# Optimization experiments

Measured on AMD Instinct MI355X. Metric: run time of the kernel, lower is better.

## Reference

```python
import jax, jax.numpy as jnp
import numpy as np

N_EMBED = 1024
HEAD_SIZE = 64


def setup_inputs() -> dict:
    key = jax.random.key(0)
    kx, kk, kq, kv = jax.random.split(key, 4)
    B, T = 8, 2048
    x = jax.random.normal(kx, (B, T, N_EMBED), dtype=jnp.float32)
    # nn.Linear weights, stored as (in, out) so projection is x @ W
    s = 1.0 / np.sqrt(N_EMBED)
    Wk = jax.random.uniform(kk, (N_EMBED, HEAD_SIZE), jnp.float32, -s, s)
    Wq = jax.random.uniform(kq, (N_EMBED, HEAD_SIZE), jnp.float32, -s, s)
    Wv = jax.random.uniform(kv, (N_EMBED, HEAD_SIZE), jnp.float32, -s, s)
    return {"x": x, "Wk": Wk, "Wq": Wq, "Wv": Wv}


def reference(x, Wk, Wq, Wv):
    # x: [B, T, C] with C = n_embed
    C = x.shape[-1]
    k = x @ Wk  # [B, T, H]
    q = x @ Wq  # [B, T, H]
    v = x @ Wv  # [B, T, H]
    # NOTE: original scales by n_embed**-0.5, not head_size**-0.5
    wei = jnp.einsum("bth,bsh->bts", q, k) * (C ** -0.5)  # [B, T, T]
    wei = jax.nn.softmax(wei, axis=-1)
    # dropout = 0.0 (eval mode) -> identity
    out = jnp.einsum("bts,bsh->bth", wei, v)  # [B, T, H]
    return out
```

## Files before the change

kernel.cpp:

```cpp
#include <hip/hip_runtime.h>
#include <stdint.h>


#define B_ 8
#define T_ 2048
#define C_ 1024
#define H_ 64

typedef float f32x4 __attribute__((ext_vector_type(4)));
typedef short s16x8 __attribute__((ext_vector_type(8)));

__device__ __forceinline__ unsigned int rhu16(float f) {
    return (__float_as_uint(f) + 0x8000u) >> 16;
}
__device__ __forceinline__ unsigned int pkbf(float lo, float hi) {
    unsigned int a = __float_as_uint(lo) + 0x8000u;
    unsigned int b = __float_as_uint(hi) + 0x8000u;
    return __builtin_amdgcn_perm(b, a, 0x07060302u);
}
__device__ __forceinline__ void ld_lds16(const void* g, void* l) {
    __builtin_amdgcn_global_load_lds(
        (const __attribute__((address_space(1))) unsigned int*)g,
        (__attribute__((address_space(3))) unsigned int*)l, 16, 0, 0);
}

__global__ __launch_bounds__(256) void wconv(const float* __restrict__ Wk,
        const float* __restrict__ Wq, const float* __restrict__ Wv,
        unsigned short* __restrict__ Wt) {
    __shared__ float ls[64 * 65];
    const int bx = blockIdx.x, t = threadIdx.x;
    const int mat = bx >> 4, c0 = (bx & 15) << 6;
    const float* W = (mat == 0) ? Wk : ((mat == 1) ? Wq : Wv);
    const float sc = (mat == 1) ? 0.03125f : 1.0f;
    #pragma unroll
    for (int k = 0; k < 4; k++) {
        int i = t + (k << 8);
        int cr = i >> 4, hq = (i & 15) << 2;
        float4 v = *reinterpret_cast<const float4*>(&W[(size_t)(c0 + cr) * H_ + hq]);
        ls[cr * 65 + hq + 0] = v.x; ls[cr * 65 + hq + 1] = v.y;
        ls[cr * 65 + hq + 2] = v.z; ls[cr * 65 + hq + 3] = v.w;
    }
    __syncthreads();
    #pragma unroll
    for (int k = 0; k < 4; k++) {
        int i = t + (k << 8);
        int h = i >> 4, cq = (i & 15) << 2;
        float a = ls[(cq + 0) * 65 + h] * sc, b = ls[(cq + 1) * 65 + h] * sc;
        float c = ls[(cq + 2) * 65 + h] * sc, d = ls[(cq + 3) * 65 + h] * sc;
        uint2 o; o.x = pkbf(a, b); o.y = pkbf(c, d);
        *reinterpret_cast<uint2*>(&Wt[(size_t)(mat * 64 + h) * C_ + c0 + cq]) = o;
    }
}

__global__ __launch_bounds__(256, 2) void qkv(const float* __restrict__ x,
        const unsigned short* __restrict__ Wt,
        unsigned short* __restrict__ kb, unsigned short* __restrict__ qb,
        unsigned short* __restrict__ vtb) {
    __shared__ __align__(16) char smem[65536];
    char* xb = smem;
    char* wb = smem + 16384;

    const int t = threadIdx.x, lane = t & 63, w = t >> 6;
    const int l15 = lane & 15, quad = lane >> 4;
    const int bx = blockIdx.x;
    const int bb = bx >> 6;
    const int mt = ((bx & 7) << 3) | ((bx >> 3) & 7);
    const int m0 = bb * T_ + mt * 32;
    const int colb = w * 48;

    size_t xg[2]; int xl[2];
    #pragma unroll
    for (int n = 0; n < 2; n++) {
        int id = w * 2 + n, rg = id >> 2, j = id & 3;
        xg[n] = (size_t)(m0 + rg * 16 + l15) * C_ + j * 16 + quad * 4;
        xl[n] = id * 1024 + lane * 16;
    }
    size_t wg[6]; int wl[6];
    #pragma unroll
    for (int n = 0; n < 6; n++) {
        int g = w * 6 + n;
        wg[n] = (size_t)(g * 8 + (lane & 7)) * C_ + (lane >> 3) * 8;
        wl[n] = g * 1024 + lane * 16;
    }

    #pragma unroll
    for (int n = 0; n < 2; n++) ld_lds16(x + xg[n], xb + xl[n]);
    #pragma unroll
    for (int n = 0; n < 6; n++) ld_lds16(Wt + wg[n], wb + wl[n]);
    __syncthreads();

    f32x4 acc[2][3];
    #pragma unroll
    for (int rt = 0; rt < 2; rt++)
        #pragma unroll
        for (int ct = 0; ct < 3; ct++)
            #pragma unroll
            for (int j = 0; j < 4; j++) acc[rt][ct][j] = 0.0f;

    #pragma unroll
    for (int i = 0; i < 16; i++) {
        const int cb = i & 1;
        const float* xc = (const float*)(xb + cb * 8192);
        const unsigned short* wc = (const unsigned short*)(wb + cb * 24576);

        float4 xr[2][2][2];
        #pragma unroll
        for (int rt = 0; rt < 2; rt++)
            #pragma unroll
            for (int ks = 0; ks < 2; ks++)
                #pragma unroll
                for (int h = 0; h < 2; h++) {
                    int c = ks * 32 + quad * 8 + h * 4;
                    int j = c >> 4, u = (c & 15) >> 2;
                    xr[rt][ks][h] = *reinterpret_cast<const float4*>(
                        xc + (rt * 4 + j) * 256 + u * 64 + l15 * 4);
                }
        s16x8 wfr[3][2];
        #pragma unroll
        for (int ct = 0; ct < 3; ct++)
            #pragma unroll
            for (int ks = 0; ks < 2; ks++) {
                int col = colb + ct * 16 + l15;
                wfr[ct][ks] = *reinterpret_cast<const s16x8*>(
                    wc + (col >> 3) * 512 + ((4 * ks + quad) * 8 + (col & 7)) * 8);
            }

        if (i < 15) {
            const int c1 = (i + 1) * 64;
            char* xn = xb + (cb ^ 1) * 8192;
            char* wn = wb + (cb ^ 1) * 24576;
            #pragma unroll
            for (int n = 0; n < 2; n++) ld_lds16(x + xg[n] + c1, xn + xl[n]);
            #pragma unroll
            for (int n = 0; n < 6; n++) ld_lds16(Wt + wg[n] + c1, wn + wl[n]);
        }

        s16x8 af[2][2];
        #pragma unroll
        for (int rt = 0; rt < 2; rt++)
            #pragma unroll
            for (int ks = 0; ks < 2; ks++) {
                const float4 a = xr[rt][ks][0], b = xr[rt][ks][1];
                uint4 pk;
                pk.x = pkbf(a.x, a.y); pk.y = pkbf(a.z, a.w);
                pk.z = pkbf(b.x, b.y); pk.w = pkbf(b.z, b.w);
                af[rt][ks] = *reinterpret_cast<s16x8*>(&pk);
            }
        #pragma unroll
        for (int ks = 0; ks < 2; ks++)
            #pragma unroll
            for (int rt = 0; rt < 2; rt++)
                #pragma unroll
                for (int ct = 0; ct < 3; ct++)
                    acc[rt][ct] = __builtin_amdgcn_mfma_f32_16x16x32_bf16(
                        af[rt][ks], wfr[ct][ks], acc[rt][ct], 0, 0, 0);
        __syncthreads();
    }

    #pragma unroll
    for (int ct = 0; ct < 3; ct++) {
        int cbv = colb + ct * 16;
        int sel = cbv >> 6;
        int h = (cbv & 63) + l15;
        #pragma unroll
        for (int rt = 0; rt < 2; rt++) {
            int row0 = m0 + rt * 16 + quad * 4;
            if (sel < 2) {
                unsigned short* dst = sel ? qb : kb;
                #pragma unroll
                for (int r = 0; r < 4; r++)
                    dst[(size_t)(row0 + r) * H_ + h] = (unsigned short)rhu16(acc[rt][ct][r]);
            } else {
                int tt = row0 - bb * T_;
                uint2 pk;
                pk.x = pkbf(acc[rt][ct][0], acc[rt][ct][1]);
                pk.y = pkbf(acc[rt][ct][2], acc[rt][ct][3]);
                *reinterpret_cast<uint2*>(&vtb[((size_t)bb * H_ + h) * T_ + tt]) = pk;
            }
        }
    }
}

__global__ __launch_bounds__(256, 2) void attn(
        const unsigned short* __restrict__ qb,
        const unsigned short* __restrict__ kb,
        const unsigned short* __restrict__ vtb,
        float* __restrict__ out) {
    __shared__ __align__(16) char smem[75776];

    const int t = threadIdx.x, lane = t & 63, w = t >> 6;
    const int l15 = lane & 15, quad = lane >> 4;
    const int bb = blockIdx.x & 7;
    const int q0 = (blockIdx.x >> 3) << 5;
    const size_t kbase = (size_t)bb * T_ * H_;
    char* Kb = smem + w * 16384;
    char* Vb = Kb + 8192;
    unsigned short* Pw = (unsigned short*)(smem + 65536 + w * 2560);

    s16x8 qf[2][2];
    #pragma unroll
    for (int rt = 0; rt < 2; rt++)
        #pragma unroll
        for (int ks = 0; ks < 2; ks++)
            qf[rt][ks] = *reinterpret_cast<const s16x8*>(
                &qb[kbase + (size_t)(q0 + rt * 16 + l15) * H_ + ks * 32 + quad * 8]);

    const unsigned short* kp = kb + kbase;
    const unsigned short* vp = vtb + (size_t)bb * H_ * T_;
    size_t kg[4], vg[4]; int kl[4], vl[4];
    #pragma unroll
    for (int g = 0; g < 4; g++) {
        kg[g] = (size_t)(g * 8 + (lane & 7)) * H_ + (lane >> 3) * 8;
        kl[g] = g * 1024 + lane * 16;
        vg[g] = (size_t)(g * 16 + l15) * T_ + quad * 8;
        vl[g] = g * 1024 + lane * 16;
    }

    const int sw = w << 9;
    #pragma unroll
    for (int g = 0; g < 4; g++) ld_lds16(kp + (size_t)sw * H_ + kg[g], Kb + kl[g]);
    #pragma unroll
    for (int g = 0; g < 4; g++) ld_lds16(vp + sw + vg[g], Vb + vl[g]);

    f32x4 oacc[2][4];
    #pragma unroll
    for (int rt = 0; rt < 2; rt++)
        #pragma unroll
        for (int ht = 0; ht < 4; ht++)
            #pragma unroll
            for (int j = 0; j < 4; j++) oacc[rt][ht][j] = 0.0f;
    float l_run[2] = {0.0f, 0.0f};
    const f32x4 z4 = {0.0f, 0.0f, 0.0f, 0.0f};

    for (int it = 0; it < 16; it++) {
        const int cb = it & 1;
        __builtin_amdgcn_s_waitcnt(0x0f70);
        const unsigned short* Kc = (const unsigned short*)(Kb + cb * 4096);
        const unsigned short* Vc = (const unsigned short*)(Vb + cb * 4096);

        s16x8 kf[2][2], vf[4];
        #pragma unroll
        for (int st = 0; st < 2; st++)
            #pragma unroll
            for (int ks = 0; ks < 2; ks++) {
                int s = st * 16 + l15;
                kf[st][ks] = *reinterpret_cast<const s16x8*>(
                    Kc + (s >> 3) * 512 + ((4 * ks + quad) * 8 + (s & 7)) * 8);
            }
        #pragma unroll
        for (int ht = 0; ht < 4; ht++)
            vf[ht] = *reinterpret_cast<const s16x8*>(
                Vc + ht * 512 + (quad * 16 + l15) * 8);

        if (it < 15) {
            const int sn = sw + (it + 1) * 32;
            char* Kn = Kb + (cb ^ 1) * 4096;
            char* Vn = Vb + (cb ^ 1) * 4096;
            #pragma unroll
            for (int g = 0; g < 4; g++) ld_lds16(kp + (size_t)sn * H_ + kg[g], Kn + kl[g]);
            #pragma unroll
            for (int g = 0; g < 4; g++) ld_lds16(vp + sn + vg[g], Vn + vl[g]);
        }

        f32x4 sacc[2][2];
        #pragma unroll
        for (int rt = 0; rt < 2; rt++)
            #pragma unroll
            for (int st = 0; st < 2; st++) {
                f32x4 s0v = __builtin_amdgcn_mfma_f32_16x16x32_bf16(kf[st][0], qf[rt][0], z4, 0, 0, 0);
                sacc[rt][st] = __builtin_amdgcn_mfma_f32_16x16x32_bf16(kf[st][1], qf[rt][1], s0v, 0, 0, 0);
            }

        #pragma unroll
        for (int rt = 0; rt < 2; rt++) {
            float ls = 0.0f;
            #pragma unroll
            for (int st = 0; st < 2; st++) {
                float p0 = __expf(sacc[rt][st][0]);
                float p1 = __expf(sacc[rt][st][1]);
                float p2 = __expf(sacc[rt][st][2]);
                float p3 = __expf(sacc[rt][st][3]);
                ls += (p0 + p1) + (p2 + p3);
                uint2 pk; pk.x = pkbf(p0, p1); pk.y = pkbf(p2, p3);
                *reinterpret_cast<uint2*>(
                    &Pw[(rt * 16 + l15) * 40 + st * 16 + quad * 4]) = pk;
            }
            l_run[rt] += ls;
        }

        #pragma unroll
        for (int rt = 0; rt < 2; rt++) {
            s16x8 pf = *reinterpret_cast<const s16x8*>(&Pw[(rt * 16 + l15) * 40 + quad * 8]);
            #pragma unroll
            for (int ht = 0; ht < 4; ht++)
                oacc[rt][ht] = __builtin_amdgcn_mfma_f32_16x16x32_bf16(
                    pf, vf[ht], oacc[rt][ht], 0, 0, 0);
        }
    }

    #pragma unroll
    for (int rt = 0; rt < 2; rt++) {
        l_run[rt] += __shfl_xor(l_run[rt], 16);
        l_run[rt] += __shfl_xor(l_run[rt], 32);
    }

    __syncthreads();
    float* Osf = (float*)smem;
    float* Ls  = (float*)smem + 3 * 32 * 66;
    if (w > 0) {
        int wi = w - 1;
        #pragma unroll
        for (int rt = 0; rt < 2; rt++) {
            if (quad == 0) Ls[wi * 32 + rt * 16 + l15] = l_run[rt];
            #pragma unroll
            for (int ht = 0; ht < 4; ht++)
                #pragma unroll
                for (int r = 0; r < 4; r++)
                    Osf[wi * 2112 + (rt * 16 + quad * 4 + r) * 66 + ht * 16 + l15] = oacc[rt][ht][r];
        }
    }
    __syncthreads();
    if (w == 0) {
        #pragma unroll
        for (int rt = 0; rt < 2; rt++)
            #pragma unroll
            for (int r = 0; r < 4; r++) {
                int row = rt * 16 + quad * 4 + r;
                float lt = __shfl(l_run[rt], quad * 4 + r)
                         + Ls[0 * 32 + row] + Ls[1 * 32 + row] + Ls[2 * 32 + row];
                float inv = 1.0f / lt;
                #pragma unroll
                for (int ht = 0; ht < 4; ht++) {
                    float o = oacc[rt][ht][r]
                            + Osf[0 * 2112 + row * 66 + ht * 16 + l15]
                            + Osf[1 * 2112 + row * 66 + ht * 16 + l15]
                            + Osf[2 * 2112 + row * 66 + ht * 16 + l15];
                    out[kbase + (size_t)(q0 + row) * H_ + ht * 16 + l15] = o * inv;
                }
            }
    }
}

extern "C" void kernel_launch(void* const* d_in, const int* in_sizes, int n_in,
                              void* d_out, int out_size, void* d_ws, size_t ws_size,
                              hipStream_t stream) {
    const float* x  = (const float*)d_in[0];
    const float* Wk = (const float*)d_in[1];
    const float* Wq = (const float*)d_in[2];
    const float* Wv = (const float*)d_in[3];

    unsigned short* kb  = (unsigned short*)d_ws;
    unsigned short* qbf = kb  + (size_t)B_ * T_ * H_;
    unsigned short* vtb = qbf + (size_t)B_ * T_ * H_;
    unsigned short* Wt  = (unsigned short*)d_out;

    wconv<<<48,  256, 0, stream>>>(Wk, Wq, Wv, Wt);
    qkv  <<<512, 256, 0, stream>>>(x, Wt, kb, qbf, vtb);
    attn <<<512, 256, 0, stream>>>(qbf, kb, vtb, (float*)d_out);
}
```

Baseline: 153.3 us.

## Load QKV operands straight to registers and issue attention prefetch earlier

The QKV projection kernel drops its LDS double buffering. It now uses 128-thread blocks where each wave computes 96 output columns, loading x rows and bf16 weight fragments from global memory straight into registers. A three-slot register prefetch ring over the x chunks replaces the per-iteration `__syncthreads`. In the attention kernel, the next K/V tile's async LDS loads are issued before the wait, and the waitcnt is relaxed to let those newer loads stay in flight, so copy overlaps compute. Trade-offs: more registers and repeated weight reads from L2 in the projection, and reliance on per-wave buffer ownership to make the reordered attention prefetch safe.

```diff
diff --git a/kernel.cpp b/kernel.cpp
--- a/kernel.cpp
+++ b/kernel.cpp
@@ -52,95 +52,76 @@
     }
 }
 
-__global__ __launch_bounds__(256, 2) void qkv(const float* __restrict__ x,
+__global__ __launch_bounds__(128, 2) void qkv(const float* __restrict__ x,
         const unsigned short* __restrict__ Wt,
         unsigned short* __restrict__ kb, unsigned short* __restrict__ qb,
         unsigned short* __restrict__ vtb) {
-    __shared__ __align__(16) char smem[65536];
-    char* xb = smem;
-    char* wb = smem + 16384;
-
     const int t = threadIdx.x, lane = t & 63, w = t >> 6;
     const int l15 = lane & 15, quad = lane >> 4;
-    const int bx = blockIdx.x;
-    const int bb = bx >> 6;
-    const int mt = ((bx & 7) << 3) | ((bx >> 3) & 7);
-    const int m0 = bb * T_ + mt * 32;
-    const int colb = w * 48;
-
-    size_t xg[2]; int xl[2];
-    #pragma unroll
-    for (int n = 0; n < 2; n++) {
-        int id = w * 2 + n, rg = id >> 2, j = id & 3;
-        xg[n] = (size_t)(m0 + rg * 16 + l15) * C_ + j * 16 + quad * 4;
-        xl[n] = id * 1024 + lane * 16;
-    }
-    size_t wg[6]; int wl[6];
-    #pragma unroll
-    for (int n = 0; n < 6; n++) {
-        int g = w * 6 + n;
-        wg[n] = (size_t)(g * 8 + (lane & 7)) * C_ + (lane >> 3) * 8;
-        wl[n] = g * 1024 + lane * 16;
-    }
-
-    #pragma unroll
-    for (int n = 0; n < 2; n++) ld_lds16(x + xg[n], xb + xl[n]);
-    #pragma unroll
-    for (int n = 0; n < 6; n++) ld_lds16(Wt + wg[n], wb + wl[n]);
-    __syncthreads();
-
-    f32x4 acc[2][3];
+    const int m0 = blockIdx.x * 32;
+    const int bb = m0 >> 11;
+    const int colw = w * 96;
+
+    const char* xq0 = (const char*)(x + (size_t)(m0 + l15) * C_ + quad * 8);
+    const char* xq1 = xq0 + (size_t)16 * C_ * 4;
+    const char* wq[6];
+    #pragma unroll
+    for (int ct = 0; ct < 6; ct++)
+        wq[ct] = (const char*)(Wt + (size_t)(colw + ct * 16 + l15) * C_ + quad * 8);
+
+    f32x4 acc[2][6];
     #pragma unroll
     for (int rt = 0; rt < 2; rt++)
         #pragma unroll
-        for (int ct = 0; ct < 3; ct++)
+        for (int ct = 0; ct < 6; ct++)
             #pragma unroll
             for (int j = 0; j < 4; j++) acc[rt][ct][j] = 0.0f;
 
-    #pragma unroll
-    for (int i = 0; i < 16; i++) {
-        const int cb = i & 1;
-        const float* xc = (const float*)(xb + cb * 8192);
-        const unsigned short* wc = (const unsigned short*)(wb + cb * 24576);
-
-        float4 xr[2][2][2];
+    float4 xr[3][2][2][2];
+    #pragma unroll
+    for (int cc = 0; cc < 2; cc++) {
+        #pragma unroll
+        for (int ks = 0; ks < 2; ks++)
+            #pragma unroll
+            for (int h = 0; h < 2; h++) {
+                xr[cc][0][ks][h] = *reinterpret_cast<const float4*>(
+                    xq0 + cc * 256 + ks * 128 + h * 16);
+                xr[cc][1][ks][h] = *reinterpret_cast<const float4*>(
+                    xq1 + cc * 256 + ks * 128 + h * 16);
+            }
+    }
+
+    #pragma unroll
+    for (int c = 0; c < 16; c++) {
+        __builtin_amdgcn_sched_barrier(0);
+        if (c < 14) {
+            const int sl = (c + 2) % 3, off = (c + 2) * 256;
+            #pragma unroll
+            for (int ks = 0; ks < 2; ks++)
+                #pragma unroll
+                for (int h = 0; h < 2; h++) {
+                    xr[sl][0][ks][h] = *reinterpret_cast<const float4*>(
+                        xq0 + off + ks * 128 + h * 16);
+                    xr[sl][1][ks][h] = *reinterpret_cast<const float4*>(
+                        xq1 + off + ks * 128 + h * 16);
+                }
+        }
+        uint4 wr[6][2];
+        #pragma unroll
+        for (int ct = 0; ct < 6; ct++)
+            #pragma unroll
+            for (int ks = 0; ks < 2; ks++)
+                wr[ct][ks] = *reinterpret_cast<const uint4*>(
+                    wq[ct] + c * 128 + ks * 64);
+        __builtin_amdgcn_sched_barrier(0);
+
+        const int cs = c % 3;
+        s16x8 af[2][2];
         #pragma unroll
         for (int rt = 0; rt < 2; rt++)
             #pragma unroll
-            for (int ks = 0; ks < 2; ks++)
-                #pragma unroll
-                for (int h = 0; h < 2; h++) {
-                    int c = ks * 32 + quad * 8 + h * 4;
-                    int j = c >> 4, u = (c & 15) >> 2;
-                    xr[rt][ks][h] = *reinterpret_cast<const float4*>(
-                        xc + (rt * 4 + j) * 256 + u * 64 + l15 * 4);
-                }
-        s16x8 wfr[3][2];
-        #pragma unroll
-        for (int ct = 0; ct < 3; ct++)
-            #pragma unroll
             for (int ks = 0; ks < 2; ks++) {
-                int col = colb + ct * 16 + l15;
-                wfr[ct][ks] = *reinterpret_cast<const s16x8*>(
-                    wc + (col >> 3) * 512 + ((4 * ks + quad) * 8 + (col & 7)) * 8);
-            }
-
-        if (i < 15) {
-            const int c1 = (i + 1) * 64;
-            char* xn = xb + (cb ^ 1) * 8192;
-            char* wn = wb + (cb ^ 1) * 24576;
-            #pragma unroll
-            for (int n = 0; n < 2; n++) ld_lds16(x + xg[n] + c1, xn + xl[n]);
-            #pragma unroll
-            for (int n = 0; n < 6; n++) ld_lds16(Wt + wg[n] + c1, wn + wl[n]);
-        }
-
-        s16x8 af[2][2];
-        #pragma unroll
-        for (int rt = 0; rt < 2; rt++)
-            #pragma unroll
-            for (int ks = 0; ks < 2; ks++) {
-                const float4 a = xr[rt][ks][0], b = xr[rt][ks][1];
+                const float4 a = xr[cs][rt][ks][0], b = xr[cs][rt][ks][1];
                 uint4 pk;
                 pk.x = pkbf(a.x, a.y); pk.y = pkbf(a.z, a.w);
                 pk.z = pkbf(b.x, b.y); pk.w = pkbf(b.z, b.w);
@@ -151,17 +132,18 @@
             #pragma unroll
             for (int rt = 0; rt < 2; rt++)
                 #pragma unroll
-                for (int ct = 0; ct < 3; ct++)
+                for (int ct = 0; ct < 6; ct++)
                     acc[rt][ct] = __builtin_amdgcn_mfma_f32_16x16x32_bf16(
-                        af[rt][ks], wfr[ct][ks], acc[rt][ct], 0, 0, 0);
-        __syncthreads();
-    }
-
-    #pragma unroll
-    for (int ct = 0; ct < 3; ct++) {
-        int cbv = colb + ct * 16;
-        int sel = cbv >> 6;
-        int h = (cbv & 63) + l15;
+                        af[rt][ks],
+                        *reinterpret_cast<s16x8*>(&wr[ct][ks]),
+                        acc[rt][ct], 0, 0, 0);
+    }
+
+    #pragma unroll
+    for (int ct = 0; ct < 6; ct++) {
+        int cb = colw + ct * 16;
+        int sel = cb >> 6;
+        int h = (cb & 63) + l15;
         #pragma unroll
         for (int rt = 0; rt < 2; rt++) {
             int row0 = m0 + rt * 16 + quad * 4;
@@ -234,7 +216,21 @@
 
     for (int it = 0; it < 16; it++) {
         const int cb = it & 1;
-        __builtin_amdgcn_s_waitcnt(0x0f70);
+        if (it < 15) {
+            const int sn = sw + (it + 1) * 32;
+            char* Kn = Kb + (cb ^ 1) * 4096;
+            char* Vn = Vb + (cb ^ 1) * 4096;
+            #pragma unroll
+            for (int g = 0; g < 4; g++) ld_lds16(kp + (size_t)sn * H_ + kg[g], Kn + kl[g]);
+            #pragma unroll
+            for (int g = 0; g < 4; g++) ld_lds16(vp + sn + vg[g], Vn + vl[g]);
+            __builtin_amdgcn_sched_barrier(0);
+            __builtin_amdgcn_s_waitcnt(0x0f78);
+        } else {
+            __builtin_amdgcn_s_waitcnt(0x0f70);
+        }
+        __builtin_amdgcn_sched_barrier(0);
+
         const unsigned short* Kc = (const unsigned short*)(Kb + cb * 4096);
         const unsigned short* Vc = (const unsigned short*)(Vb + cb * 4096);
 
@@ -251,16 +247,6 @@
         for (int ht = 0; ht < 4; ht++)
             vf[ht] = *reinterpret_cast<const s16x8*>(
                 Vc + ht * 512 + (quad * 16 + l15) * 8);
-
-        if (it < 15) {
-            const int sn = sw + (it + 1) * 32;
-            char* Kn = Kb + (cb ^ 1) * 4096;
-            char* Vn = Vb + (cb ^ 1) * 4096;
-            #pragma unroll
-            for (int g = 0; g < 4; g++) ld_lds16(kp + (size_t)sn * H_ + kg[g], Kn + kl[g]);
-            #pragma unroll
-            for (int g = 0; g < 4; g++) ld_lds16(vp + sn + vg[g], Vn + vl[g]);
-        }
 
         f32x4 sacc[2][2];
         #pragma unroll
@@ -355,6 +341,6 @@
     unsigned short* Wt  = (unsigned short*)d_out;
 
     wconv<<<48,  256, 0, stream>>>(Wk, Wq, Wv, Wt);
-    qkv  <<<512, 256, 0, stream>>>(x, Wt, kb, qbf, vtb);
+    qkv  <<<512, 128, 0, stream>>>(x, Wt, kb, qbf, vtb);
     attn <<<512, 256, 0, stream>>>(qbf, kb, vtb, (float*)d_out);
 }
```

Result: slower. 160.5 us (+4.7%).

## Double waves per block in qkv and attn; load K/V fragments directly from global

Applied to the files above, without the earlier changes.

Both qkv and attn now launch 512-thread blocks with 8 waves, and each wave handles one 16-row tile instead of two. This halves per-wave registers and raises occupancy. In attn, the LDS double-buffered K/V staging is dropped: each wave reads its K and V^T fragments straight from global memory (through cache), so shared memory shrinks to the P scratch and the reduction buffers. This trades explicit async prefetch for more waves to hide latency, at the risk of exposed global-load latency. Each K/V fragment is now read by two waves, which doubles L2 traffic.

```diff
diff --git a/kernel.cpp b/kernel.cpp
--- a/kernel.cpp
+++ b/kernel.cpp
@@ -52,7 +52,7 @@
     }
 }
 
-__global__ __launch_bounds__(256, 2) void qkv(const float* __restrict__ x,
+__global__ __launch_bounds__(512, 4) void qkv(const float* __restrict__ x,
         const unsigned short* __restrict__ Wt,
         unsigned short* __restrict__ kb, unsigned short* __restrict__ qb,
         unsigned short* __restrict__ vtb) {
@@ -61,60 +61,57 @@
     char* wb = smem + 16384;
 
     const int t = threadIdx.x, lane = t & 63, w = t >> 6;
+    const int rw = w >> 2, cw = w & 3;
     const int l15 = lane & 15, quad = lane >> 4;
-    const int bx = blockIdx.x;
-    const int bb = bx >> 6;
-    const int mt = ((bx & 7) << 3) | ((bx >> 3) & 7);
-    const int m0 = bb * T_ + mt * 32;
-    const int colb = w * 48;
-
-    size_t xg[2]; int xl[2];
-    #pragma unroll
-    for (int n = 0; n < 2; n++) {
-        int id = w * 2 + n, rg = id >> 2, j = id & 3;
-        xg[n] = (size_t)(m0 + rg * 16 + l15) * C_ + j * 16 + quad * 4;
-        xl[n] = id * 1024 + lane * 16;
-    }
-    size_t wg[6]; int wl[6];
-    #pragma unroll
-    for (int n = 0; n < 6; n++) {
-        int g = w * 6 + n;
+    const int m0 = blockIdx.x * 32;
+    const int bb = m0 >> 11;
+    const int colb = cw * 48;
+
+    const size_t xg = (size_t)(m0 + (w >> 2) * 16 + l15) * C_ + (w & 3) * 16 + quad * 4;
+    const int    xl = w * 1024 + lane * 16;
+    size_t wg[3]; int wl[3];
+    #pragma unroll
+    for (int n = 0; n < 3; n++) {
+        int g = w * 3 + n;
         wg[n] = (size_t)(g * 8 + (lane & 7)) * C_ + (lane >> 3) * 8;
         wl[n] = g * 1024 + lane * 16;
     }
 
-    #pragma unroll
-    for (int n = 0; n < 2; n++) ld_lds16(x + xg[n], xb + xl[n]);
-    #pragma unroll
-    for (int n = 0; n < 6; n++) ld_lds16(Wt + wg[n], wb + wl[n]);
-    __syncthreads();
-
-    f32x4 acc[2][3];
-    #pragma unroll
-    for (int rt = 0; rt < 2; rt++)
-        #pragma unroll
-        for (int ct = 0; ct < 3; ct++)
-            #pragma unroll
-            for (int j = 0; j < 4; j++) acc[rt][ct][j] = 0.0f;
-
-    #pragma unroll
+    ld_lds16(x + xg, xb + xl);
+    #pragma unroll
+    for (int n = 0; n < 3; n++) ld_lds16(Wt + wg[n], wb + wl[n]);
+    __syncthreads();
+
+    f32x4 acc[3];
+    #pragma unroll
+    for (int ct = 0; ct < 3; ct++)
+        #pragma unroll
+        for (int j = 0; j < 4; j++) acc[ct][j] = 0.0f;
+
     for (int i = 0; i < 16; i++) {
         const int cb = i & 1;
         const float* xc = (const float*)(xb + cb * 8192);
         const unsigned short* wc = (const unsigned short*)(wb + cb * 24576);
 
-        float4 xr[2][2][2];
-        #pragma unroll
-        for (int rt = 0; rt < 2; rt++)
-            #pragma unroll
-            for (int ks = 0; ks < 2; ks++)
-                #pragma unroll
-                for (int h = 0; h < 2; h++) {
-                    int c = ks * 32 + quad * 8 + h * 4;
-                    int j = c >> 4, u = (c & 15) >> 2;
-                    xr[rt][ks][h] = *reinterpret_cast<const float4*>(
-                        xc + (rt * 4 + j) * 256 + u * 64 + l15 * 4);
-                }
+        if (i < 15) {
+            const int c1 = (i + 1) * 64;
+            char* xn = xb + (cb ^ 1) * 8192;
+            char* wn = wb + (cb ^ 1) * 24576;
+            ld_lds16(x + xg + c1, xn + xl);
+            #pragma unroll
+            for (int n = 0; n < 3; n++) ld_lds16(Wt + wg[n] + c1, wn + wl[n]);
+        }
+
+        float4 xr[2][2];
+        #pragma unroll
+        for (int ks = 0; ks < 2; ks++)
+            #pragma unroll
+            for (int h = 0; h < 2; h++) {
+                int c = ks * 32 + quad * 8 + h * 4;
+                int j = c >> 4, u = (c & 15) >> 2;
+                xr[ks][h] = *reinterpret_cast<const float4*>(
+                    xc + (rw * 4 + j) * 256 + u * 64 + l15 * 4);
+            }
         s16x8 wfr[3][2];
         #pragma unroll
         for (int ct = 0; ct < 3; ct++)
@@ -125,35 +122,21 @@
                     wc + (col >> 3) * 512 + ((4 * ks + quad) * 8 + (col & 7)) * 8);
             }
 
-        if (i < 15) {
-            const int c1 = (i + 1) * 64;
-            char* xn = xb + (cb ^ 1) * 8192;
-            char* wn = wb + (cb ^ 1) * 24576;
-            #pragma unroll
-            for (int n = 0; n < 2; n++) ld_lds16(x + xg[n] + c1, xn + xl[n]);
-            #pragma unroll
-            for (int n = 0; n < 6; n++) ld_lds16(Wt + wg[n] + c1, wn + wl[n]);
-        }
-
-        s16x8 af[2][2];
-        #pragma unroll
-        for (int rt = 0; rt < 2; rt++)
-            #pragma unroll
-            for (int ks = 0; ks < 2; ks++) {
-                const float4 a = xr[rt][ks][0], b = xr[rt][ks][1];
-                uint4 pk;
-                pk.x = pkbf(a.x, a.y); pk.y = pkbf(a.z, a.w);
-                pk.z = pkbf(b.x, b.y); pk.w = pkbf(b.z, b.w);
-                af[rt][ks] = *reinterpret_cast<s16x8*>(&pk);
-            }
+        s16x8 af[2];
+        #pragma unroll
+        for (int ks = 0; ks < 2; ks++) {
+            const float4 a = xr[ks][0], b = xr[ks][1];
+            uint4 pk;
+            pk.x = pkbf(a.x, a.y); pk.y = pkbf(a.z, a.w);
+            pk.z = pkbf(b.x, b.y); pk.w = pkbf(b.z, b.w);
+            af[ks] = *reinterpret_cast<s16x8*>(&pk);
+        }
         #pragma unroll
         for (int ks = 0; ks < 2; ks++)
             #pragma unroll
-            for (int rt = 0; rt < 2; rt++)
-                #pragma unroll
-                for (int ct = 0; ct < 3; ct++)
-                    acc[rt][ct] = __builtin_amdgcn_mfma_f32_16x16x32_bf16(
-                        af[rt][ks], wfr[ct][ks], acc[rt][ct], 0, 0, 0);
+            for (int ct = 0; ct < 3; ct++)
+                acc[ct] = __builtin_amdgcn_mfma_f32_16x16x32_bf16(
+                    af[ks], wfr[ct][ks], acc[ct], 0, 0, 0);
         __syncthreads();
     }
 
@@ -162,182 +145,135 @@
         int cbv = colb + ct * 16;
         int sel = cbv >> 6;
         int h = (cbv & 63) + l15;
-        #pragma unroll
-        for (int rt = 0; rt < 2; rt++) {
-            int row0 = m0 + rt * 16 + quad * 4;
-            if (sel < 2) {
-                unsigned short* dst = sel ? qb : kb;
-                #pragma unroll
-                for (int r = 0; r < 4; r++)
-                    dst[(size_t)(row0 + r) * H_ + h] = (unsigned short)rhu16(acc[rt][ct][r]);
-            } else {
-                int tt = row0 - bb * T_;
-                uint2 pk;
-                pk.x = pkbf(acc[rt][ct][0], acc[rt][ct][1]);
-                pk.y = pkbf(acc[rt][ct][2], acc[rt][ct][3]);
-                *reinterpret_cast<uint2*>(&vtb[((size_t)bb * H_ + h) * T_ + tt]) = pk;
-            }
-        }
-    }
-}
-
-__global__ __launch_bounds__(256, 2) void attn(
+        int row0 = m0 + rw * 16 + quad * 4;
+        if (sel < 2) {
+            unsigned short* dst = sel ? qb : kb;
+            #pragma unroll
+            for (int r = 0; r < 4; r++)
+                dst[(size_t)(row0 + r) * H_ + h] = (unsigned short)rhu16(acc[ct][r]);
+        } else {
+            int tt = row0 - bb * T_;
+            uint2 pk;
+            pk.x = pkbf(acc[ct][0], acc[ct][1]);
+            pk.y = pkbf(acc[ct][2], acc[ct][3]);
+            *reinterpret_cast<uint2*>(&vtb[((size_t)bb * H_ + h) * T_ + tt]) = pk;
+        }
+    }
+}
+
+__global__ __launch_bounds__(512, 4) void attn(
         const unsigned short* __restrict__ qb,
         const unsigned short* __restrict__ kb,
         const unsigned short* __restrict__ vtb,
         float* __restrict__ out) {
-    __shared__ __align__(16) char smem[75776];
+    __shared__ __align__(16) char smem[25728];
 
     const int t = threadIdx.x, lane = t & 63, w = t >> 6;
+    const int rt = w >> 2, sq = w & 3;
     const int l15 = lane & 15, quad = lane >> 4;
     const int bb = blockIdx.x & 7;
     const int q0 = (blockIdx.x >> 3) << 5;
     const size_t kbase = (size_t)bb * T_ * H_;
-    char* Kb = smem + w * 16384;
-    char* Vb = Kb + 8192;
-    unsigned short* Pw = (unsigned short*)(smem + 65536 + w * 2560);
-
-    s16x8 qf[2][2];
-    #pragma unroll
-    for (int rt = 0; rt < 2; rt++)
-        #pragma unroll
-        for (int ks = 0; ks < 2; ks++)
-            qf[rt][ks] = *reinterpret_cast<const s16x8*>(
-                &qb[kbase + (size_t)(q0 + rt * 16 + l15) * H_ + ks * 32 + quad * 8]);
-
-    const unsigned short* kp = kb + kbase;
-    const unsigned short* vp = vtb + (size_t)bb * H_ * T_;
-    size_t kg[4], vg[4]; int kl[4], vl[4];
-    #pragma unroll
-    for (int g = 0; g < 4; g++) {
-        kg[g] = (size_t)(g * 8 + (lane & 7)) * H_ + (lane >> 3) * 8;
-        kl[g] = g * 1024 + lane * 16;
-        vg[g] = (size_t)(g * 16 + l15) * T_ + quad * 8;
-        vl[g] = g * 1024 + lane * 16;
-    }
-
-    const int sw = w << 9;
-    #pragma unroll
-    for (int g = 0; g < 4; g++) ld_lds16(kp + (size_t)sw * H_ + kg[g], Kb + kl[g]);
-    #pragma unroll
-    for (int g = 0; g < 4; g++) ld_lds16(vp + sw + vg[g], Vb + vl[g]);
-
-    f32x4 oacc[2][4];
-    #pragma unroll
-    for (int rt = 0; rt < 2; rt++)
+    unsigned short* Pw = (unsigned short*)(smem + w * 1280);
+
+    s16x8 qf[2];
+    #pragma unroll
+    for (int ks = 0; ks < 2; ks++)
+        qf[ks] = *reinterpret_cast<const s16x8*>(
+            &qb[kbase + (size_t)(q0 + rt * 16 + l15) * H_ + ks * 32 + quad * 8]);
+
+    const int sw = sq << 9;
+    const unsigned short* kq = kb + kbase + (size_t)(sw + l15) * H_ + quad * 8;
+    const unsigned short* vq[4];
+    #pragma unroll
+    for (int ht = 0; ht < 4; ht++)
+        vq[ht] = vtb + ((size_t)bb * H_ + ht * 16 + l15) * T_ + sw + quad * 8;
+
+    f32x4 oacc[4];
+    #pragma unroll
+    for (int ht = 0; ht < 4; ht++)
+        #pragma unroll
+        for (int j = 0; j < 4; j++) oacc[ht][j] = 0.0f;
+    float l_run = 0.0f;
+    const f32x4 z4 = {0.0f, 0.0f, 0.0f, 0.0f};
+
+    for (int it = 0; it < 16; it++) {
+        s16x8 kf[2][2], vf[4];
+        #pragma unroll
+        for (int st = 0; st < 2; st++)
+            #pragma unroll
+            for (int ks = 0; ks < 2; ks++)
+                kf[st][ks] = *reinterpret_cast<const s16x8*>(
+                    kq + (size_t)(it * 32 + st * 16) * H_ + ks * 32);
         #pragma unroll
         for (int ht = 0; ht < 4; ht++)
-            #pragma unroll
-            for (int j = 0; j < 4; j++) oacc[rt][ht][j] = 0.0f;
-    float l_run[2] = {0.0f, 0.0f};
-    const f32x4 z4 = {0.0f, 0.0f, 0.0f, 0.0f};
-
-    for (int it = 0; it < 16; it++) {
-        const int cb = it & 1;
-        __builtin_amdgcn_s_waitcnt(0x0f70);
-        const unsigned short* Kc = (const unsigned short*)(Kb + cb * 4096);
-        const unsigned short* Vc = (const unsigned short*)(Vb + cb * 4096);
-
-        s16x8 kf[2][2], vf[4];
-        #pragma unroll
-        for (int st = 0; st < 2; st++)
-            #pragma unroll
-            for (int ks = 0; ks < 2; ks++) {
-                int s = st * 16 + l15;
-                kf[st][ks] = *reinterpret_cast<const s16x8*>(
-                    Kc + (s >> 3) * 512 + ((4 * ks + quad) * 8 + (s & 7)) * 8);
+            vf[ht] = *reinterpret_cast<const s16x8*>(vq[ht] + it * 32);
+
+        f32x4 sacc[2];
+        #pragma unroll
+        for (int st = 0; st < 2; st++) {
+            f32x4 s0v = __builtin_amdgcn_mfma_f32_16x16x32_bf16(
+                kf[st][0], qf[0], z4, 0, 0, 0);
+            sacc[st] = __builtin_amdgcn_mfma_f32_16x16x32_bf16(
+                kf[st][1], qf[1], s0v, 0, 0, 0);
+        }
+
+        float ls = 0.0f;
+        #pragma unroll
+        for (int st = 0; st < 2; st++) {
+            float p0 = __expf(sacc[st][0]);
+            float p1 = __expf(sacc[st][1]);
+            float p2 = __expf(sacc[st][2]);
+            float p3 = __expf(sacc[st][3]);
+            ls += (p0 + p1) + (p2 + p3);
+            uint2 pk; pk.x = pkbf(p0, p1); pk.y = pkbf(p2, p3);
+            *reinterpret_cast<uint2*>(&Pw[l15 * 40 + st * 16 + quad * 4]) = pk;
+        }
+        l_run += ls;
+
+        s16x8 pf = *reinterpret_cast<const s16x8*>(&Pw[l15 * 40 + quad * 8]);
+        #pragma unroll
+        for (int ht = 0; ht < 4; ht++)
+            oacc[ht] = __builtin_amdgcn_mfma_f32_16x16x32_bf16(
+                pf, vf[ht], oacc[ht], 0, 0, 0);
+    }
+
+    l_run += __shfl_xor(l_run, 16);
+    l_run += __shfl_xor(l_run, 32);
+
+    __syncthreads();
+    float* Osf = (float*)smem;
+    float* Ls  = (float*)(smem + 25344);
+    if (sq > 0) {
+        int si = sq - 1;
+        if (quad == 0) Ls[(rt * 3 + si) * 16 + l15] = l_run;
+        #pragma unroll
+        for (int ht = 0; ht < 4; ht++)
+            #pragma unroll
+            for (int r = 0; r < 4; r++)
+                Osf[((rt * 3 + si) * 16 + quad * 4 + r) * 66 + ht * 16 + l15] =
+                    oacc[ht][r];
+    }
+    __syncthreads();
+    if (sq == 0) {
+        #pragma unroll
+        for (int r = 0; r < 4; r++) {
+            int row = quad * 4 + r;
+            float lt = __shfl(l_run, row)
+                     + Ls[(rt * 3 + 0) * 16 + row]
+                     + Ls[(rt * 3 + 1) * 16 + row]
+                     + Ls[(rt * 3 + 2) * 16 + row];
+            float inv = 1.0f / lt;
+            #pragma unroll
+            for (int ht = 0; ht < 4; ht++) {
+                float o = oacc[ht][r]
+                        + Osf[((rt * 3 + 0) * 16 + row) * 66 + ht * 16 + l15]
+                        + Osf[((rt * 3 + 1) * 16 + row) * 66 + ht * 16 + l15]
+                        + Osf[((rt * 3 + 2) * 16 + row) * 66 + ht * 16 + l15];
+                out[kbase + (size_t)(q0 + rt * 16 + row) * H_ + ht * 16 + l15] =
+                    o * inv;
             }
-        #pragma unroll
-        for (int ht = 0; ht < 4; ht++)
-            vf[ht] = *reinterpret_cast<const s16x8*>(
-                Vc + ht * 512 + (quad * 16 + l15) * 8);
-
-        if (it < 15) {
-            const int sn = sw + (it + 1) * 32;
-            char* Kn = Kb + (cb ^ 1) * 4096;
-            char* Vn = Vb + (cb ^ 1) * 4096;
-            #pragma unroll
-            for (int g = 0; g < 4; g++) ld_lds16(kp + (size_t)sn * H_ + kg[g], Kn + kl[g]);
-            #pragma unroll
-            for (int g = 0; g < 4; g++) ld_lds16(vp + sn + vg[g], Vn + vl[g]);
-        }
-
-        f32x4 sacc[2][2];
-        #pragma unroll
-        for (int rt = 0; rt < 2; rt++)
-            #pragma unroll
-            for (int st = 0; st < 2; st++) {
-                f32x4 s0v = __builtin_amdgcn_mfma_f32_16x16x32_bf16(kf[st][0], qf[rt][0], z4, 0, 0, 0);
-                sacc[rt][st] = __builtin_amdgcn_mfma_f32_16x16x32_bf16(kf[st][1], qf[rt][1], s0v, 0, 0, 0);
-            }
-
-        #pragma unroll
-        for (int rt = 0; rt < 2; rt++) {
-            float ls = 0.0f;
-            #pragma unroll
-            for (int st = 0; st < 2; st++) {
-                float p0 = __expf(sacc[rt][st][0]);
-                float p1 = __expf(sacc[rt][st][1]);
-                float p2 = __expf(sacc[rt][st][2]);
-                float p3 = __expf(sacc[rt][st][3]);
-                ls += (p0 + p1) + (p2 + p3);
-                uint2 pk; pk.x = pkbf(p0, p1); pk.y = pkbf(p2, p3);
-                *reinterpret_cast<uint2*>(
-                    &Pw[(rt * 16 + l15) * 40 + st * 16 + quad * 4]) = pk;
-            }
-            l_run[rt] += ls;
-        }
-
-        #pragma unroll
-        for (int rt = 0; rt < 2; rt++) {
-            s16x8 pf = *reinterpret_cast<const s16x8*>(&Pw[(rt * 16 + l15) * 40 + quad * 8]);
-            #pragma unroll
-            for (int ht = 0; ht < 4; ht++)
-                oacc[rt][ht] = __builtin_amdgcn_mfma_f32_16x16x32_bf16(
-                    pf, vf[ht], oacc[rt][ht], 0, 0, 0);
-        }
-    }
-
-    #pragma unroll
-    for (int rt = 0; rt < 2; rt++) {
-        l_run[rt] += __shfl_xor(l_run[rt], 16);
-        l_run[rt] += __shfl_xor(l_run[rt], 32);
-    }
-
-    __syncthreads();
-    float* Osf = (float*)smem;
-    float* Ls  = (float*)smem + 3 * 32 * 66;
-    if (w > 0) {
-        int wi = w - 1;
-        #pragma unroll
-        for (int rt = 0; rt < 2; rt++) {
-            if (quad == 0) Ls[wi * 32 + rt * 16 + l15] = l_run[rt];
-            #pragma unroll
-            for (int ht = 0; ht < 4; ht++)
-                #pragma unroll
-                for (int r = 0; r < 4; r++)
-                    Osf[wi * 2112 + (rt * 16 + quad * 4 + r) * 66 + ht * 16 + l15] = oacc[rt][ht][r];
-        }
-    }
-    __syncthreads();
-    if (w == 0) {
-        #pragma unroll
-        for (int rt = 0; rt < 2; rt++)
-            #pragma unroll
-            for (int r = 0; r < 4; r++) {
-                int row = rt * 16 + quad * 4 + r;
-                float lt = __shfl(l_run[rt], quad * 4 + r)
-                         + Ls[0 * 32 + row] + Ls[1 * 32 + row] + Ls[2 * 32 + row];
-                float inv = 1.0f / lt;
-                #pragma unroll
-                for (int ht = 0; ht < 4; ht++) {
-                    float o = oacc[rt][ht][r]
-                            + Osf[0 * 2112 + row * 66 + ht * 16 + l15]
-                            + Osf[1 * 2112 + row * 66 + ht * 16 + l15]
-                            + Osf[2 * 2112 + row * 66 + ht * 16 + l15];
-                    out[kbase + (size_t)(q0 + row) * H_ + ht * 16 + l15] = o * inv;
-                }
-            }
+        }
     }
 }
 
@@ -355,6 +291,6 @@
     unsigned short* Wt  = (unsigned short*)d_out;
 
     wconv<<<48,  256, 0, stream>>>(Wk, Wq, Wv, Wt);
-    qkv  <<<512, 256, 0, stream>>>(x, Wt, kb, qbf, vtb);
-    attn <<<512, 256, 0, stream>>>(qbf, kb, vtb, (float*)d_out);
-}
+    qkv  <<<512, 512, 0, stream>>>(x, Wt, kb, qbf, vtb);
+    attn <<<512, 512, 0, stream>>>(qbf, kb, vtb, (float*)d_out);
+}
```

Measured after the change: 181.5 us. +18.4%, slower.

## Load K/V fragments directly from global memory with 64-key tiles, dropping LDS staging

Applied to the files above, without the earlier changes.

The attention kernel stops staging K and V through double-buffered LDS via global_load_lds. Each wave now reads its MFMA K and V fragments straight from global memory into registers. The key tile per iteration doubles from 32 to 64 (8 iterations instead of 16), and the P scratch buffer is enlarged to match. Shared memory shrinks from about 74KB to 25KB, which could allow more resident blocks, at the cost of losing explicit prefetch overlap and relying on L2 and cache for the K/V reuse across blocks.

```diff
diff --git a/kernel.cpp b/kernel.cpp
--- a/kernel.cpp
+++ b/kernel.cpp
@@ -186,16 +186,14 @@
         const unsigned short* __restrict__ kb,
         const unsigned short* __restrict__ vtb,
         float* __restrict__ out) {
-    __shared__ __align__(16) char smem[75776];
+    __shared__ __align__(16) char smem[25728];
 
     const int t = threadIdx.x, lane = t & 63, w = t >> 6;
     const int l15 = lane & 15, quad = lane >> 4;
     const int bb = blockIdx.x & 7;
     const int q0 = (blockIdx.x >> 3) << 5;
     const size_t kbase = (size_t)bb * T_ * H_;
-    char* Kb = smem + w * 16384;
-    char* Vb = Kb + 8192;
-    unsigned short* Pw = (unsigned short*)(smem + 65536 + w * 2560);
+    unsigned short* Pw = (unsigned short*)(smem + w * 4608);
 
     s16x8 qf[2][2];
     #pragma unroll
@@ -205,22 +203,12 @@
             qf[rt][ks] = *reinterpret_cast<const s16x8*>(
                 &qb[kbase + (size_t)(q0 + rt * 16 + l15) * H_ + ks * 32 + quad * 8]);
 
-    const unsigned short* kp = kb + kbase;
-    const unsigned short* vp = vtb + (size_t)bb * H_ * T_;
-    size_t kg[4], vg[4]; int kl[4], vl[4];
-    #pragma unroll
-    for (int g = 0; g < 4; g++) {
-        kg[g] = (size_t)(g * 8 + (lane & 7)) * H_ + (lane >> 3) * 8;
-        kl[g] = g * 1024 + lane * 16;
-        vg[g] = (size_t)(g * 16 + l15) * T_ + quad * 8;
-        vl[g] = g * 1024 + lane * 16;
-    }
-
     const int sw = w << 9;
-    #pragma unroll
-    for (int g = 0; g < 4; g++) ld_lds16(kp + (size_t)sw * H_ + kg[g], Kb + kl[g]);
-    #pragma unroll
-    for (int g = 0; g < 4; g++) ld_lds16(vp + sw + vg[g], Vb + vl[g]);
+    const unsigned short* kq = kb + kbase + (size_t)(sw + l15) * H_ + quad * 8;
+    const unsigned short* vq[4];
+    #pragma unroll
+    for (int ht = 0; ht < 4; ht++)
+        vq[ht] = vtb + ((size_t)bb * H_ + ht * 16 + l15) * T_ + sw + quad * 8;
 
     f32x4 oacc[2][4];
     #pragma unroll
@@ -232,50 +220,37 @@
     float l_run[2] = {0.0f, 0.0f};
     const f32x4 z4 = {0.0f, 0.0f, 0.0f, 0.0f};
 
-    for (int it = 0; it < 16; it++) {
-        const int cb = it & 1;
-        __builtin_amdgcn_s_waitcnt(0x0f70);
-        const unsigned short* Kc = (const unsigned short*)(Kb + cb * 4096);
-        const unsigned short* Vc = (const unsigned short*)(Vb + cb * 4096);
-
-        s16x8 kf[2][2], vf[4];
-        #pragma unroll
-        for (int st = 0; st < 2; st++)
-            #pragma unroll
-            for (int ks = 0; ks < 2; ks++) {
-                int s = st * 16 + l15;
+    for (int it = 0; it < 8; it++) {
+        s16x8 kf[4][2], vf[2][4];
+        #pragma unroll
+        for (int st = 0; st < 4; st++)
+            #pragma unroll
+            for (int ks = 0; ks < 2; ks++)
                 kf[st][ks] = *reinterpret_cast<const s16x8*>(
-                    Kc + (s >> 3) * 512 + ((4 * ks + quad) * 8 + (s & 7)) * 8);
-            }
-        #pragma unroll
-        for (int ht = 0; ht < 4; ht++)
-            vf[ht] = *reinterpret_cast<const s16x8*>(
-                Vc + ht * 512 + (quad * 16 + l15) * 8);
-
-        if (it < 15) {
-            const int sn = sw + (it + 1) * 32;
-            char* Kn = Kb + (cb ^ 1) * 4096;
-            char* Vn = Vb + (cb ^ 1) * 4096;
-            #pragma unroll
-            for (int g = 0; g < 4; g++) ld_lds16(kp + (size_t)sn * H_ + kg[g], Kn + kl[g]);
-            #pragma unroll
-            for (int g = 0; g < 4; g++) ld_lds16(vp + sn + vg[g], Vn + vl[g]);
-        }
-
-        f32x4 sacc[2][2];
-        #pragma unroll
-        for (int rt = 0; rt < 2; rt++)
-            #pragma unroll
-            for (int st = 0; st < 2; st++) {
-                f32x4 s0v = __builtin_amdgcn_mfma_f32_16x16x32_bf16(kf[st][0], qf[rt][0], z4, 0, 0, 0);
-                sacc[rt][st] = __builtin_amdgcn_mfma_f32_16x16x32_bf16(kf[st][1], qf[rt][1], s0v, 0, 0, 0);
+                    kq + (size_t)(it * 64 + st * 16) * H_ + ks * 32);
+        #pragma unroll
+        for (int ks2 = 0; ks2 < 2; ks2++)
+            #pragma unroll
+            for (int ht = 0; ht < 4; ht++)
+                vf[ks2][ht] = *reinterpret_cast<const s16x8*>(
+                    vq[ht] + it * 64 + ks2 * 32);
+
+        f32x4 sacc[2][4];
+        #pragma unroll
+        for (int rt = 0; rt < 2; rt++)
+            #pragma unroll
+            for (int st = 0; st < 4; st++) {
+                f32x4 s0v = __builtin_amdgcn_mfma_f32_16x16x32_bf16(
+                    kf[st][0], qf[rt][0], z4, 0, 0, 0);
+                sacc[rt][st] = __builtin_amdgcn_mfma_f32_16x16x32_bf16(
+                    kf[st][1], qf[rt][1], s0v, 0, 0, 0);
             }
 
         #pragma unroll
         for (int rt = 0; rt < 2; rt++) {
             float ls = 0.0f;
             #pragma unroll
-            for (int st = 0; st < 2; st++) {
+            for (int st = 0; st < 4; st++) {
                 float p0 = __expf(sacc[rt][st][0]);
                 float p1 = __expf(sacc[rt][st][1]);
                 float p2 = __expf(sacc[rt][st][2]);
@@ -283,19 +258,22 @@
                 ls += (p0 + p1) + (p2 + p3);
                 uint2 pk; pk.x = pkbf(p0, p1); pk.y = pkbf(p2, p3);
                 *reinterpret_cast<uint2*>(
-                    &Pw[(rt * 16 + l15) * 40 + st * 16 + quad * 4]) = pk;
+                    &Pw[(rt * 16 + l15) * 72 + st * 16 + quad * 4]) = pk;
             }
             l_run[rt] += ls;
         }
 
         #pragma unroll
-        for (int rt = 0; rt < 2; rt++) {
-            s16x8 pf = *reinterpret_cast<const s16x8*>(&Pw[(rt * 16 + l15) * 40 + quad * 8]);
-            #pragma unroll
-            for (int ht = 0; ht < 4; ht++)
-                oacc[rt][ht] = __builtin_amdgcn_mfma_f32_16x16x32_bf16(
-                    pf, vf[ht], oacc[rt][ht], 0, 0, 0);
-        }
+        for (int rt = 0; rt < 2; rt++)
+            #pragma unroll
+            for (int ks2 = 0; ks2 < 2; ks2++) {
+                s16x8 pf = *reinterpret_cast<const s16x8*>(
+                    &Pw[(rt * 16 + l15) * 72 + ks2 * 32 + quad * 8]);
+                #pragma unroll
+                for (int ht = 0; ht < 4; ht++)
+                    oacc[rt][ht] = __builtin_amdgcn_mfma_f32_16x16x32_bf16(
+                        pf, vf[ks2][ht], oacc[rt][ht], 0, 0, 0);
+            }
     }
 
     #pragma unroll
```

New measurement: 151.7 us. Within noise of the previous version (-1.1%).
